# Kernel tuning notes

Hardware: AMD Instinct MI355X
Metric: run time of the kernel (lower is better)

Reference implementation:

```python
import jax, jax.numpy as jnp
import numpy as np

M, K, N = 32768, 2048, 2048  # tokens, in_features, out_features
QMIN, QMAX = -128, 127


def setup_inputs() -> dict:
    key = jax.random.key(0)
    ks = jax.random.split(key, 7)
    x = jax.random.normal(ks[0], (M, K), dtype=jnp.float32).astype(jnp.float16)
    int_weight = jax.random.randint(ks[1], (N, K), QMIN, QMAX + 1, dtype=jnp.int32).astype(jnp.int8)
    # calibrated-looking asymmetric activation quant params (fp16 buffers, [num_steps]=1)
    act_delta = (jax.random.uniform(ks[2], (1,), dtype=jnp.float32) * 0.02 + 0.005).astype(jnp.float16)
    act_zp = jnp.round(jax.random.normal(ks[3], (1,), dtype=jnp.float32) * 8.0).astype(jnp.float16)
    # per-output-channel weight scales; fuse precomputed dequant buffers consistently
    w_delta = jax.random.uniform(ks[4], (N,), dtype=jnp.float32) * 0.002 + 1e-4
    act_times_weight_delta = (act_delta.astype(jnp.float32) * w_delta)[None, :]  # [1, N]
    w_row_sum = jnp.sum(int_weight.astype(jnp.float32), axis=1)  # [N]
    zp_times_weight_channel_sum = (act_zp.astype(jnp.float32) * w_row_sum * act_times_weight_delta[0])[None, :]  # [1, N]
    bias = jax.random.normal(ks[5], (N,), dtype=jnp.float32) * 0.02
    return {
        "input": x,
        "act_delta": act_delta,
        "act_zp": act_zp,
        "zp_times_weight_channel_sum": zp_times_weight_channel_sum,
        "act_times_weight_delta": act_times_weight_delta,
        "bias": bias,
        "int_weight": int_weight,
    }


def reference(input, act_delta, act_zp, zp_times_weight_channel_sum,
              act_times_weight_delta, bias, int_weight):
    # current_step == num_steps - 1 == 0
    delta = act_delta[0].astype(jnp.float32)
    zp = act_zp[0].astype(jnp.float32)
    atwd = act_times_weight_delta[0]            # [N] = act_delta * weight_delta
    zp_sum = zp_times_weight_channel_sum[0]     # [N] = zp * rowsum(W_int) * atwd
    # asymmetric int8 activation quantization: q = clip(round(x/delta + zp))
    q = jnp.clip(jnp.round(input.astype(jnp.float32) / delta + zp), QMIN, QMAX).astype(jnp.int8)
    # int8 GEMM with int32 accumulation: [M,K] x [K,N]
    acc = jnp.matmul(q.astype(jnp.int32), int_weight.astype(jnp.int32).T)
    # fused dequant + zero-point correction + bias, cast to fp16
    out = acc.astype(jnp.float32) * atwd - zp_sum + bias
    return out.astype(jnp.float16)
```

## Files before the change

kernel.cpp:

```cpp
#include <hip/hip_runtime.h>
#include <hip/hip_fp16.h>
#include <stdint.h>

typedef int i32x4 __attribute__((ext_vector_type(4)));

#define BM 128
#define BN 256
#define BKB 64
#define NSLOT 3
#define SLOT_BYTES 24576
#define THREADS 512

__device__ __forceinline__ void gload_lds16(const void* g, void* l) {
  __builtin_amdgcn_global_load_lds(
      (const __attribute__((address_space(1))) unsigned int*)g,
      (__attribute__((address_space(3))) unsigned int*)l, 16, 0, 0);
}

__global__ __launch_bounds__(256) void quant_x_kernel(
    const float* __restrict__ x, const float* __restrict__ deltap,
    const float* __restrict__ zpp, int8_t* __restrict__ q, int n16) {
  const float rdelta = 1.0f / deltap[0];
  const float zp = zpp[0];
  for (int i = blockIdx.x * blockDim.x + threadIdx.x; i < n16;
       i += gridDim.x * blockDim.x) {
    const float4* src = (const float4*)x + (size_t)i * 4;
    int packed[4];
#pragma unroll
    for (int g = 0; g < 4; ++g) {
      float4 v = src[g];
      float f0 = fminf(127.f, fmaxf(-128.f, rintf(fmaf(v.x, rdelta, zp))));
      float f1 = fminf(127.f, fmaxf(-128.f, rintf(fmaf(v.y, rdelta, zp))));
      float f2 = fminf(127.f, fmaxf(-128.f, rintf(fmaf(v.z, rdelta, zp))));
      float f3 = fminf(127.f, fmaxf(-128.f, rintf(fmaf(v.w, rdelta, zp))));
      int q0 = (int)f0 & 255, q1 = (int)f1 & 255, q2 = (int)f2 & 255, q3 = (int)f3 & 255;
      packed[g] = q0 | (q1 << 8) | (q2 << 16) | (q3 << 24);
    }
    ((int4*)q)[i] = make_int4(packed[0], packed[1], packed[2], packed[3]);
  }
}

__global__ __launch_bounds__(256) void pack_w_kernel(
    const int* __restrict__ w, int8_t* __restrict__ wp, int n16) {
  int i = blockIdx.x * blockDim.x + threadIdx.x;
  if (i >= n16) return;
  const int4* src = (const int4*)w + (size_t)i * 4;
  int packed[4];
#pragma unroll
  for (int g = 0; g < 4; ++g) {
    int4 v = src[g];
    packed[g] = (v.x & 255) | ((v.y & 255) << 8) | ((v.z & 255) << 16) | ((v.w & 255) << 24);
  }
  ((int4*)wp)[i] = make_int4(packed[0], packed[1], packed[2], packed[3]);
}

__global__ __launch_bounds__(THREADS, 4) void gemm_i8_kernel(
    const int8_t* __restrict__ Aq, const int8_t* __restrict__ Bw,
    const float* __restrict__ atwd, const float* __restrict__ zpws,
    const float* __restrict__ bias, float* __restrict__ out,
    int Mc, int Nc, int Kc) {
  __shared__ int8_t lds[NSLOT * SLOT_BYTES];

  const int nwg = gridDim.x;
  int bid = blockIdx.x;
  if ((nwg & 7) == 0) bid = (bid & 7) * (nwg >> 3) + (bid >> 3);
  const int nbn = Nc / BN;
  const int bm = bid / nbn;
  const int bn = bid % nbn;

  const int tid = threadIdx.x;
  const size_t K = (size_t)Kc;
  const int NT = Kc / BKB;

  const int srow = tid >> 2;
  const int lc = (tid & 3) ^ ((tid >> 3) & 3);
  const int8_t* gA = Aq + ((size_t)(bm * BM + srow)) * K + lc * 16;
  const int8_t* gB = Bw + ((size_t)(bn * BN + srow)) * K + lc * 16;
  const size_t bHalf = (size_t)128 * K;
  int8_t* ldst = &lds[tid * 16];

  auto stage = [&](int t, int slot) {
    int8_t* l = ldst + slot * SLOT_BYTES;
    const size_t koff = (size_t)t * BKB;
    gload_lds16(gA + koff, l);
    gload_lds16(gB + koff, l + 8192);
    gload_lds16(gB + koff + bHalf, l + 16384);
  };

  const int lane = tid & 63;
  const int wave = tid >> 6;
  const int wr = wave >> 2;
  const int wc = wave & 3;
  const int fr = lane & 15;
  const int kc = lane >> 4;
  const int coff = ((kc ^ ((fr >> 1) & 3)) << 4);
  const int aRow = wr * 64 + fr;
  const int bRow = wc * 64 + fr;

  i32x4 acc[4][4] = {};

  stage(0, 0);
  if (NT > 1) stage(1, 1);
  if (NT > 1) asm volatile("s_waitcnt vmcnt(3)" ::: "memory");
  else        asm volatile("s_waitcnt vmcnt(0)" ::: "memory");
  __builtin_amdgcn_s_barrier();
  __builtin_amdgcn_sched_barrier(0);

  int rs = 0;
  for (int t = 0; t < NT; ++t) {
    const int8_t* sA = &lds[rs * SLOT_BYTES];
    const int8_t* sB = sA + 8192;

    i32x4 afr[4], bfr[4];
#pragma unroll
    for (int j = 0; j < 4; ++j)
      bfr[j] = *(const i32x4*)&sB[(bRow + j * 16) * 64 + coff];
#pragma unroll
    for (int i = 0; i < 4; ++i)
      afr[i] = *(const i32x4*)&sA[(aRow + i * 16) * 64 + coff];

    if (t + 2 < NT) {
      int ws = rs + 2; if (ws >= NSLOT) ws -= NSLOT;
      stage(t + 2, ws);
    }

#pragma unroll
    for (int i = 0; i < 4; ++i)
#pragma unroll
      for (int j = 0; j < 4; ++j)
        acc[i][j] = __builtin_amdgcn_mfma_i32_16x16x64_i8(afr[i], bfr[j], acc[i][j], 0, 0, 0);

    if (t < NT - 1) {
      if (t + 2 < NT) asm volatile("s_waitcnt vmcnt(3)" ::: "memory");
      else            asm volatile("s_waitcnt vmcnt(0)" ::: "memory");
      __builtin_amdgcn_s_barrier();
      __builtin_amdgcn_sched_barrier(0);
    }
    rs = rs + 1; if (rs >= NSLOT) rs -= NSLOT;
  }

  const int r4 = (lane >> 4) << 2;
  const int cn0 = bn * BN + wc * 64 + fr;
  float aw4[4], zs4[4], bs4[4];
#pragma unroll
  for (int j = 0; j < 4; ++j) {
    aw4[j] = atwd[cn0 + j * 16];
    zs4[j] = zpws[cn0 + j * 16];
    bs4[j] = bias[cn0 + j * 16];
  }
#pragma unroll
  for (int mi = 0; mi < 4; ++mi) {
#pragma unroll
    for (int r = 0; r < 4; ++r) {
      const size_t rbase = (size_t)(bm * BM + wr * 64 + mi * 16 + r4 + r) * (size_t)Nc;
#pragma unroll
      for (int j = 0; j < 4; ++j) {
        float v = (float)acc[mi][j][r] * aw4[j] - zs4[j] + bs4[j];
        v = __half2float(__float2half(v));
        out[rbase + cn0 + j * 16] = v;
      }
    }
  }
}

extern "C" void kernel_launch(void* const* d_in, const int* in_sizes, int n_in,
                              void* d_out, int out_size, void* d_ws, size_t ws_size,
                              hipStream_t stream) {
  const float* x         = (const float*)d_in[0];
  const float* act_delta = (const float*)d_in[1];
  const float* act_zp    = (const float*)d_in[2];
  const float* zpws      = (const float*)d_in[3];
  const float* atwd      = (const float*)d_in[4];
  const float* bias      = (const float*)d_in[5];
  const int*   w32       = (const int*)d_in[6];
  float* out = (float*)d_out;

  const int N = in_sizes[5];
  const int K = in_sizes[6] / N;
  const int M = in_sizes[0] / K;

  int8_t* q  = (int8_t*)d_ws;
  int8_t* wp = q + (size_t)M * K;

  {
    int n16 = (M * K) / 16;
    int grid = (n16 + 255) / 256;
    if (grid > 2048) grid = 2048;
    quant_x_kernel<<<grid, 256, 0, stream>>>(x, act_delta, act_zp, q, n16);
  }
  {
    int n16 = (N * K) / 16;
    pack_w_kernel<<<(n16 + 255) / 256, 256, 0, stream>>>(w32, wp, n16);
  }
  {
    dim3 grid((M / BM) * (N / BN));
    gemm_i8_kernel<<<grid, THREADS, 0, stream>>>(q, wp, atwd, zpws, bias, out, M, N, K);
  }
}
```

Baseline: 247.4 us.

## Enlarge GEMM tile to 256x256x128 with double-buffered LDS and 8-chunk swizzle

Doubles the M tile to 256 and the K step to 128, so each wave computes an 8x4 grid of MFMA fragments. The shared-memory pipeline moves from three 24KB slots to two 64KB slots, with a full vmcnt(0) wait each iteration and an XOR swizzle over 8 16-byte chunks. The goal is higher arithmetic intensity per LDS and global byte and fewer barriers per unit of work. In exchange, 128KB of LDS per block and many more accumulator registers (occupancy bound 2) cut concurrency, and prefetch depth drops to one stage.

Result: no change. 245.8 us (-0.6%).

```diff
diff --git a/kernel.cpp b/kernel.cpp
--- a/kernel.cpp
+++ b/kernel.cpp
@@ -4,11 +4,10 @@
 
 typedef int i32x4 __attribute__((ext_vector_type(4)));
 
-#define BM 128
+#define BM 256
 #define BN 256
-#define BKB 64
-#define NSLOT 3
-#define SLOT_BYTES 24576
+#define BKB 128
+#define SLOT 65536
 #define THREADS 512
 
 __device__ __forceinline__ void gload_lds16(const void* g, void* l) {
@@ -54,12 +53,12 @@
   ((int4*)wp)[i] = make_int4(packed[0], packed[1], packed[2], packed[3]);
 }
 
-__global__ __launch_bounds__(THREADS, 4) void gemm_i8_kernel(
+__global__ __launch_bounds__(THREADS, 2) void gemm_i8_kernel(
     const int8_t* __restrict__ Aq, const int8_t* __restrict__ Bw,
     const float* __restrict__ atwd, const float* __restrict__ zpws,
     const float* __restrict__ bias, float* __restrict__ out,
     int Mc, int Nc, int Kc) {
-  __shared__ int8_t lds[NSLOT * SLOT_BYTES];
+  __shared__ int8_t lds[2 * SLOT];
 
   const int nwg = gridDim.x;
   int bid = blockIdx.x;
@@ -72,19 +71,23 @@
   const size_t K = (size_t)Kc;
   const int NT = Kc / BKB;
 
-  const int srow = tid >> 2;
-  const int lc = (tid & 3) ^ ((tid >> 3) & 3);
-  const int8_t* gA = Aq + ((size_t)(bm * BM + srow)) * K + lc * 16;
-  const int8_t* gB = Bw + ((size_t)(bn * BN + srow)) * K + lc * 16;
-  const size_t bHalf = (size_t)128 * K;
+  const int srow = tid >> 3;
+  const int cs = tid & 7;
+  const int cl = cs ^ (srow & 7);
+  const int8_t* gA = Aq + ((size_t)(bm * BM + srow)) * K + cl * 16;
+  const int8_t* gB = Bw + ((size_t)(bn * BN + srow)) * K + cl * 16;
+  const size_t row64 = (size_t)64 * K;
   int8_t* ldst = &lds[tid * 16];
 
   auto stage = [&](int t, int slot) {
-    int8_t* l = ldst + slot * SLOT_BYTES;
+    int8_t* l = ldst + slot * SLOT;
     const size_t koff = (size_t)t * BKB;
-    gload_lds16(gA + koff, l);
-    gload_lds16(gB + koff, l + 8192);
-    gload_lds16(gB + koff + bHalf, l + 16384);
+#pragma unroll
+    for (int r = 0; r < 4; ++r)
+      gload_lds16(gA + koff + r * row64, l + r * 8192);
+#pragma unroll
+    for (int r = 0; r < 4; ++r)
+      gload_lds16(gB + koff + r * row64, l + 32768 + r * 8192);
   };
 
   const int lane = tid & 63;
@@ -93,50 +96,49 @@
   const int wc = wave & 3;
   const int fr = lane & 15;
   const int kc = lane >> 4;
-  const int coff = ((kc ^ ((fr >> 1) & 3)) << 4);
-  const int aRow = wr * 64 + fr;
+  const int swz = fr & 7;
+  const int aRow = wr * 128 + fr;
   const int bRow = wc * 64 + fr;
 
-  i32x4 acc[4][4] = {};
+  i32x4 acc[8][4] = {};
 
   stage(0, 0);
-  if (NT > 1) stage(1, 1);
-  if (NT > 1) asm volatile("s_waitcnt vmcnt(3)" ::: "memory");
-  else        asm volatile("s_waitcnt vmcnt(0)" ::: "memory");
+  asm volatile("s_waitcnt vmcnt(0)" ::: "memory");
   __builtin_amdgcn_s_barrier();
   __builtin_amdgcn_sched_barrier(0);
 
-  int rs = 0;
   for (int t = 0; t < NT; ++t) {
-    const int8_t* sA = &lds[rs * SLOT_BYTES];
-    const int8_t* sB = sA + 8192;
-
-    i32x4 afr[4], bfr[4];
-#pragma unroll
-    for (int j = 0; j < 4; ++j)
-      bfr[j] = *(const i32x4*)&sB[(bRow + j * 16) * 64 + coff];
-#pragma unroll
-    for (int i = 0; i < 4; ++i)
-      afr[i] = *(const i32x4*)&sA[(aRow + i * 16) * 64 + coff];
-
-    if (t + 2 < NT) {
-      int ws = rs + 2; if (ws >= NSLOT) ws -= NSLOT;
-      stage(t + 2, ws);
-    }
-
-#pragma unroll
-    for (int i = 0; i < 4; ++i)
+    const int8_t* sA = &lds[(t & 1) * SLOT];
+    const int8_t* sB = sA + 32768;
+
+    i32x4 af[8][2], bf[4][2];
+#pragma unroll
+    for (int ks = 0; ks < 2; ++ks) {
+      const int co = ((ks * 4 + kc) ^ swz) << 4;
 #pragma unroll
       for (int j = 0; j < 4; ++j)
-        acc[i][j] = __builtin_amdgcn_mfma_i32_16x16x64_i8(afr[i], bfr[j], acc[i][j], 0, 0, 0);
+        bf[j][ks] = *(const i32x4*)&sB[(bRow + j * 16) * 128 + co];
+#pragma unroll
+      for (int i = 0; i < 8; ++i)
+        af[i][ks] = *(const i32x4*)&sA[(aRow + ((i & 3) * 16) + ((i >> 2) * 64)) * 128 + co];
+    }
+
+    if (t + 1 < NT) stage(t + 1, (t + 1) & 1);
+
+#pragma unroll
+    for (int ks = 0; ks < 2; ++ks)
+#pragma unroll
+      for (int i = 0; i < 8; ++i)
+#pragma unroll
+        for (int j = 0; j < 4; ++j)
+          acc[i][j] = __builtin_amdgcn_mfma_i32_16x16x64_i8(
+              af[((i >> 2) * 4) + (i & 3)][ks], bf[j][ks], acc[i][j], 0, 0, 0);
 
     if (t < NT - 1) {
-      if (t + 2 < NT) asm volatile("s_waitcnt vmcnt(3)" ::: "memory");
-      else            asm volatile("s_waitcnt vmcnt(0)" ::: "memory");
+      asm volatile("s_waitcnt vmcnt(0)" ::: "memory");
       __builtin_amdgcn_s_barrier();
       __builtin_amdgcn_sched_barrier(0);
     }
-    rs = rs + 1; if (rs >= NSLOT) rs -= NSLOT;
   }
 
   const int r4 = (lane >> 4) << 2;
@@ -149,13 +151,14 @@
     bs4[j] = bias[cn0 + j * 16];
   }
 #pragma unroll
-  for (int mi = 0; mi < 4; ++mi) {
+  for (int i = 0; i < 8; ++i) {
+    const int mrow = ((i & 3) * 16) + ((i >> 2) * 64);
 #pragma unroll
     for (int r = 0; r < 4; ++r) {
-      const size_t rbase = (size_t)(bm * BM + wr * 64 + mi * 16 + r4 + r) * (size_t)Nc;
+      const size_t rbase = (size_t)(bm * BM + wr * 128 + mrow + r4 + r) * (size_t)Nc;
 #pragma unroll
       for (int j = 0; j < 4; ++j) {
-        float v = (float)acc[mi][j][r] * aw4[j] - zs4[j] + bs4[j];
+        float v = (float)acc[i][j][r] * aw4[j] - zs4[j] + bs4[j];
         v = __half2float(__float2half(v));
         out[rbase + cn0 + j * 16] = v;
       }
```
